# Optimization experiments

Measured on AMD Instinct MI355X. Metric: run time of the kernel, lower is better.

The kernel has to match this reference:

```python
import jax, jax.numpy as jnp
import numpy as np

EPS = 1e-08


def setup_inputs() -> dict:
    key = jax.random.key(0)
    k1, k2 = jax.random.split(key)
    N, D, C = 8192, 512, 1000
    features = jax.random.uniform(k1, (N, D), dtype=jnp.float32)
    logits = jax.random.normal(k2, (N, C), dtype=jnp.float32)
    return {"features": features, "logits": logits}


def reference(features, logits):
    N = features.shape[0]
    # softmax over classes, plus eps (matches F.softmax(...) + eps)
    p = jax.nn.softmax(logits, axis=1) + EPS                     # [N, C]
    # similarity matrix with diagonal removed
    cos_sim = features @ features.T - jnp.eye(N, dtype=features.dtype)  # [N, N]
    neighbor_mask = (cos_sim >= -1).astype(cos_sim.dtype)
    w = cos_sim * neighbor_mask
    w = w / jnp.sum(w, axis=1, keepdims=True)                    # row-normalized weights
    weighted_sum_nb = w @ p                                      # [N, C]
    # F.kl_div(log_input, target, reduction='batchmean')
    # = sum(target * (log(target) - log_input)) / N
    kl = jnp.sum(weighted_sum_nb * (jnp.log(weighted_sum_nb) - jnp.log(p))) / N
    return kl
```

## Files before the change

kernel.cpp:

```cpp
#include <hip/hip_runtime.h>
#include <math.h>

#define NN 8192
#define DD 512
#define CC 1000
#define CP 1024
#define CPD (CP*DD)

typedef __attribute__((ext_vector_type(8))) short short8;
typedef __attribute__((ext_vector_type(4))) float f32x4;
typedef __attribute__((ext_vector_type(4))) unsigned short us4;
typedef __attribute__((ext_vector_type(8))) unsigned short us8;
typedef __attribute__((ext_vector_type(4))) unsigned int ui4;

__device__ __forceinline__ float bf2f(unsigned short u){
  union{unsigned int i; float f;} v; v.i = ((unsigned int)u)<<16; return v.f;
}
__device__ __forceinline__ unsigned short f2bf(float f){
  union{float f; unsigned int i;} v; v.f = f;
  unsigned int r = v.i + 0x7FFF + ((v.i>>16)&1);
  return (unsigned short)(r>>16);
}
__device__ __forceinline__ float waveRedSum(float v){
  #pragma unroll
  for(int o=32;o;o>>=1) v += __shfl_xor(v,o,64);
  return v;
}
__device__ __forceinline__ float waveRedMax(float v){
  #pragma unroll
  for(int o=32;o;o>>=1) v = fmaxf(v,__shfl_xor(v,o,64));
  return v;
}
__device__ __forceinline__ void gload_lds16(const void* g, void* l){
  __builtin_amdgcn_global_load_lds((const __attribute__((address_space(1))) void*)g,
                                   (__attribute__((address_space(3))) void*)l, 16, 0, 0);
}

__global__ __launch_bounds__(256) void k_prep(const float* __restrict__ F,
                                              const float* __restrict__ L,
                                              unsigned short* __restrict__ FbT,
                                              unsigned short* __restrict__ Fb,
                                              float* __restrict__ gpart,
                                              unsigned short* __restrict__ PbT){
  __shared__ __align__(16) char smem[8*1028*4];
  int bid = blockIdx.x;
  int grp = bid/3, r = bid - grp*3;
  int t = threadIdx.x;

  if(r < 2){
    int cb = grp*2 + r;
    unsigned short* lds = (unsigned short*)smem;
    float* gq = (float*)(smem + 64*68*2);
    int i0 = (cb & 127)*64, d0 = (cb >> 7)*64;
    int cx = t&15, ry = t>>4;
    float ca0=0.f,ca1=0.f,ca2=0.f,ca3=0.f;
    #pragma unroll
    for(int rr=0;rr<4;rr++){
      int row = rr*16 + ry;
      f32x4 fv = *(const f32x4*)&F[(size_t)(i0+row)*DD + d0 + cx*4];
      us4 u; u[0]=f2bf(fv[0]); u[1]=f2bf(fv[1]); u[2]=f2bf(fv[2]); u[3]=f2bf(fv[3]);
      *(us4*)&lds[row*68 + cx*4] = u;
      *(us4*)&Fb[(size_t)(i0+row)*DD + d0 + cx*4] = u;
      ca0+=fv[0]; ca1+=fv[1]; ca2+=fv[2]; ca3+=fv[3];
    }
    {
      f32x4 cv; cv[0]=ca0; cv[1]=ca1; cv[2]=ca2; cv[3]=ca3;
      *(f32x4*)&gq[ry*64 + cx*4] = cv;
    }
    __syncthreads();
    #pragma unroll
    for(int rr=0;rr<4;rr++){
      int d = rr*16 + ry;
      us4 u;
      #pragma unroll
      for(int q=0;q<4;q++) u[q] = lds[(cx*4+q)*68 + d];
      *(us4*)&FbT[(size_t)(d0+d)*NN + i0 + cx*4] = u;
    }
    __syncthreads();
    if(t<64){
      float s=0.f;
      #pragma unroll
      for(int j=0;j<16;j++) s += gq[j*64+t];
      gpart[(cb&127)*DD + d0 + t] = s;
    }
  } else {
    int sb = grp;
    unsigned int (*lt)[1028] = (unsigned int(*)[1028])smem;
    int l = t&63, w = t>>6;
    int i0 = sb*16;
    #pragma unroll
    for(int q=0;q<4;q++){
      int rr = w*4 + q;
      int row = i0 + rr;
      const float* lr = L + (size_t)row*CC;
      float v[16]; float mx = -1e30f;
      #pragma unroll
      for(int k=0;k<16;k++){ int c = l + 64*k; v[k] = (c<CC)? lr[c] : -1e30f; mx = fmaxf(mx,v[k]); }
      mx = waveRedMax(mx);
      float s = 0.f;
      #pragma unroll
      for(int k=0;k<16;k++){ v[k] = __expf(v[k]-mx); s += v[k]; }
      s = waveRedSum(s);
      float inv = 1.0f/s;
      #pragma unroll
      for(int k=0;k<16;k++){
        int c = l + 64*k;
        float p = v[k]*inv + 1e-8f;
        unsigned short h = (c<CC)? f2bf(p) : (unsigned short)0;
        *((unsigned short*)&lt[rr>>1][c] + (rr&1)) = h;
      }
    }
    __syncthreads();
    #pragma unroll
    for(int k=0;k<4;k++){
      int c = t + 256*k;
      ui4 a, b;
      #pragma unroll
      for(int j=0;j<4;j++){ a[j] = lt[j][c]; b[j] = lt[j+4][c]; }
      *(ui4*)&PbT[(size_t)c*NN + i0]     = a;
      *(ui4*)&PbT[(size_t)c*NN + i0 + 8] = b;
    }
  }
}

__global__ __launch_bounds__(256,2) void k_gemm1(const unsigned short* __restrict__ A,
                                                 const unsigned short* __restrict__ B,
                                                 unsigned short* __restrict__ Tpb,
                                                 const float* __restrict__ gpart,
                                                 float* __restrict__ g){
  __shared__ unsigned short Al[128*64];
  __shared__ unsigned short Bl[128*64];
  __shared__ float rs[4][64];
  int bid = blockIdx.x;
  int t = threadIdx.x;
  if(bid < 8){
    int d = bid*64 + (t&63);
    int q = t>>6;
    float s = 0.f;
    #pragma unroll
    for(int j=0;j<32;j++) s += gpart[(size_t)(q*32+j)*DD + d];
    rs[q][t&63] = s;
    __syncthreads();
    if(q==0) g[d] = rs[0][t&63]+rs[1][t&63]+rs[2][t&63]+rs[3][t&63];
    return;
  }
  int gb = bid - 8;
  int Lsw = (gb&7)*64 + (gb>>3);
  int l = t&63, w = t>>6;
  int bx = Lsw & 7, by = (Lsw>>3) & 3, bz = Lsw>>5;
  int m0 = bx*128, n0 = by*128;
  int k0 = bz*512;
  int wm = w>>1, wn = w&1;
  f32x4 acc[4][4] = {};
  int srow = w*32 + (l>>3);
  int scl  = (l&7) ^ (srow&7);
  const unsigned short* Ab = A + (size_t)(m0 + srow)*NN + k0 + scl*8;
  const unsigned short* Bb = B + (size_t)(n0 + srow)*NN + k0 + scl*8;
  unsigned short* AlB = Al + (w*32)*64;
  unsigned short* BlB = Bl + (w*32)*64;

  for(int kt=0; kt<512; kt+=64){
    __syncthreads();
    #pragma unroll
    for(int q=0;q<4;q++){
      gload_lds16(Ab + (size_t)q*8*NN + kt, AlB + q*8*64);
      gload_lds16(Bb + (size_t)q*8*NN + kt, BlB + q*8*64);
    }
    asm volatile("s_waitcnt vmcnt(0)" ::: "memory");
    __syncthreads();
    #pragma unroll
    for(int ks=0;ks<2;ks++){
      short8 af[4], bf[4];
      #pragma unroll
      for(int mi=0;mi<4;mi++){
        int rr = wm*64 + mi*16 + (l&15);
        int ch = ((ks<<2) + (l>>4)) ^ (rr&7);
        af[mi] = *(const short8*)&Al[rr*64 + ch*8];
      }
      #pragma unroll
      for(int ni=0;ni<4;ni++){
        int rr = wn*64 + ni*16 + (l&15);
        int ch = ((ks<<2) + (l>>4)) ^ (rr&7);
        bf[ni] = *(const short8*)&Bl[rr*64 + ch*8];
      }
      #pragma unroll
      for(int mi=0;mi<4;mi++)
        #pragma unroll
        for(int ni=0;ni<4;ni++)
          acc[mi][ni] = __builtin_amdgcn_mfma_f32_16x16x32_bf16(af[mi], bf[ni], acc[mi][ni], 0,0,0);
    }
  }
  unsigned short* Tz = Tpb + (size_t)bz*CPD;
  int rbase = (l>>4)*4;
  #pragma unroll
  for(int mi=0;mi<4;mi++){
    int c = m0 + wm*64 + mi*16 + rbase;
    #pragma unroll
    for(int ni=0;ni<4;ni++){
      int d = n0 + wn*64 + ni*16 + (l&15);
      #pragma unroll
      for(int j=0;j<4;j++)
        Tz[(size_t)(c+j)*DD + d] = f2bf(acc[mi][ni][j]);
    }
  }
}

__global__ __launch_bounds__(256) void k_redT(const unsigned short* __restrict__ Tpb,
                                              const unsigned short* __restrict__ Fb,
                                              const float* __restrict__ g,
                                              unsigned short* __restrict__ Ttb,
                                              float* __restrict__ invr){
  int t = threadIdx.x;
  size_t i = ((size_t)blockIdx.x*256 + (size_t)t)*8;
  f32x4 s0 = {0.f,0.f,0.f,0.f}, s1 = {0.f,0.f,0.f,0.f};
  #pragma unroll
  for(int z=0;z<16;z++){
    us8 v = *(const us8*)&Tpb[(size_t)z*CPD + i];
    s0[0]+=bf2f(v[0]); s0[1]+=bf2f(v[1]); s0[2]+=bf2f(v[2]); s0[3]+=bf2f(v[3]);
    s1[0]+=bf2f(v[4]); s1[1]+=bf2f(v[5]); s1[2]+=bf2f(v[6]); s1[3]+=bf2f(v[7]);
  }
  us8 u;
  u[0]=f2bf(s0[0]); u[1]=f2bf(s0[1]); u[2]=f2bf(s0[2]); u[3]=f2bf(s0[3]);
  u[4]=f2bf(s1[0]); u[5]=f2bf(s1[1]); u[6]=f2bf(s1[2]); u[7]=f2bf(s1[3]);
  *(us8*)&Ttb[i] = u;
  int row = blockIdx.x*32 + (t>>3);
  int seg = (t&7)*64;
  const unsigned short* fr = Fb + (size_t)row*DD + seg;
  const float* gr = g + seg;
  float s = 0.f;
  #pragma unroll
  for(int j=0;j<8;j++){
    us8 f8 = *(const us8*)&fr[j*8];
    f32x4 ga = *(const f32x4*)&gr[j*8];
    f32x4 gb = *(const f32x4*)&gr[j*8+4];
    s += bf2f(f8[0])*ga[0]+bf2f(f8[1])*ga[1]+bf2f(f8[2])*ga[2]+bf2f(f8[3])*ga[3]
       + bf2f(f8[4])*gb[0]+bf2f(f8[5])*gb[1]+bf2f(f8[6])*gb[2]+bf2f(f8[7])*gb[3];
  }
  s += __shfl_xor(s,1,64); s += __shfl_xor(s,2,64); s += __shfl_xor(s,4,64);
  if((t&7)==0) invr[row] = 1.0f/(s - 1.0f);
}

__global__ __launch_bounds__(256,2) void k_gemm2(const unsigned short* __restrict__ Fb,
                                                 const unsigned short* __restrict__ Bt,
                                                 const unsigned short* __restrict__ PbT,
                                                 const float* __restrict__ invr,
                                                 float* __restrict__ partials){
  __shared__ __align__(16) unsigned short smem[128*136];
  __shared__ float red[4];
  unsigned short* Al = smem;
  unsigned short* Bl = smem + 128*64;
  int bid = blockIdx.x;
  int Lsw = (bid&7)*64 + (bid>>3);
  int t = threadIdx.x, l = t&63, w = t>>6;
  int m0 = (Lsw>>3)*128, n0 = (Lsw&7)*128;
  int wm = w>>1, wn = w&1;
  f32x4 acc[4][4] = {};
  int srow = w*32 + (l>>3);
  int scl  = (l&7) ^ (srow&7);
  const unsigned short* Ab = Fb + (size_t)(m0 + srow)*DD + scl*8;
  const unsigned short* Bb = Bt + (size_t)(n0 + srow)*DD + scl*8;
  unsigned short* AlB = Al + (w*32)*64;
  unsigned short* BlB = Bl + (w*32)*64;

  for(int kt=0; kt<512; kt+=64){
    __syncthreads();
    #pragma unroll
    for(int q=0;q<4;q++){
      gload_lds16(Ab + (size_t)q*8*DD + kt, AlB + q*8*64);
      gload_lds16(Bb + (size_t)q*8*DD + kt, BlB + q*8*64);
    }
    asm volatile("s_waitcnt vmcnt(0)" ::: "memory");
    __syncthreads();
    #pragma unroll
    for(int ks=0;ks<2;ks++){
      short8 af[4], bf[4];
      #pragma unroll
      for(int mi=0;mi<4;mi++){
        int rr = wm*64 + mi*16 + (l&15);
        int ch = ((ks<<2) + (l>>4)) ^ (rr&7);
        af[mi] = *(const short8*)&Al[rr*64 + ch*8];
      }
      #pragma unroll
      for(int ni=0;ni<4;ni++){
        int rr = wn*64 + ni*16 + (l&15);
        int ch = ((ks<<2) + (l>>4)) ^ (rr&7);
        bf[ni] = *(const short8*)&Bl[rr*64 + ch*8];
      }
      #pragma unroll
      for(int mi=0;mi<4;mi++)
        #pragma unroll
        for(int ni=0;ni<4;ni++)
          acc[mi][ni] = __builtin_amdgcn_mfma_f32_16x16x32_bf16(af[mi], bf[ni], acc[mi][ni], 0,0,0);
    }
  }
  __syncthreads();
  #pragma unroll
  for(int j=0;j<8;j++){
    int e = j*256 + t;
    int row = e >> 4;
    int ch  = e & 15;
    us8 v = *(const us8*)&PbT[(size_t)(n0+row)*NN + m0 + ch*8];
    *(us8*)&smem[row*136 + ch*8] = v;
  }
  __syncthreads();
  float kl = 0.f;
  int rbase = (l>>4)*4;
  #pragma unroll
  for(int mi=0;mi<4;mi++){
    int i_base = m0 + wm*64 + mi*16 + rbase;
    int ci = wm*64 + mi*16 + rbase;
    f32x4 ir4 = *(const f32x4*)&invr[i_base];
    #pragma unroll
    for(int ni=0;ni<4;ni++){
      int cr = wn*64 + ni*16 + (l&15);
      int c = n0 + cr;
      if(c < CC){
        us4 p4 = *(const us4*)&smem[cr*136 + ci];
        #pragma unroll
        for(int j=0;j<4;j++){
          float p = bf2f(p4[j]);
          float ws = (acc[mi][ni][j] - p) * ir4[j];
          kl += ws * (__logf(ws) - __logf(p));
        }
      }
    }
  }
  kl = waveRedSum(kl);
  if(l==0) red[w]=kl;
  __syncthreads();
  if(t==0) partials[Lsw] = red[0]+red[1]+red[2]+red[3];
}

__global__ __launch_bounds__(64) void k_finalize(const float* __restrict__ partials,
                                                 float* __restrict__ out){
  int l = threadIdx.x;
  double s = 0.0;
  for(int j=l; j<512; j+=64) s += (double)partials[j];
  #pragma unroll
  for(int o=32;o;o>>=1) s += __shfl_xor(s,o,64);
  if(l==0) out[0] = (float)(s / (double)NN);
}

extern "C" void kernel_launch(void* const* d_in, const int* in_sizes, int n_in,
                              void* d_out, int out_size, void* d_ws, size_t ws_size,
                              hipStream_t stream){
  const float* F = (const float*)d_in[0];
  const float* L = (const float*)d_in[1];
  float* out = (float*)d_out;

  unsigned char* w8 = (unsigned char*)d_ws;
  unsigned short* FbT = (unsigned short*)w8;
  unsigned short* PbT = (unsigned short*)(w8 + (8u<<20));
  unsigned short* Tpb = (unsigned short*)(w8 + (24u<<20));
  unsigned short* Ttb = (unsigned short*)(w8 + (40u<<20));
  unsigned short* Fb  = (unsigned short*)(w8 + (41u<<20));
  float* gpart        = (float*)(w8 + (49u<<20));
  float* g            = (float*)(w8 + (49u<<20) + 262144);
  float* invr         = (float*)(w8 + (49u<<20) + 264192);
  float* partials     = (float*)(w8 + (49u<<20) + 296960);

  hipLaunchKernelGGL(k_prep,     dim3(1536),   dim3(256), 0, stream, F, L, FbT, Fb, gpart, PbT);
  hipLaunchKernelGGL(k_gemm1,    dim3(520),    dim3(256), 0, stream, PbT, FbT, Tpb, gpart, g);
  hipLaunchKernelGGL(k_redT,     dim3(256),    dim3(256), 0, stream, Tpb, Fb, g, Ttb, invr);
  hipLaunchKernelGGL(k_gemm2,    dim3(512),    dim3(256), 0, stream, Fb, Ttb, PbT, invr, partials);
  hipLaunchKernelGGL(k_finalize, dim3(1),      dim3(64),  0, stream, partials, out);
}
```

Measured before the change: 67.94 us.

## Double-buffer LDS tiles in both GEMM kernels to overlap loads with MFMA

Both GEMM kernels now use two LDS buffers and prefetch the next K tile from global memory into the spare buffer while MFMAs run on the current one. A partial vmcnt wait lets the current tile's loads complete while the next tile's loads stay in flight. This is meant to hide global-to-LDS latency that the old load-wait-compute loop exposed. LDS use per block doubles to 64KB, which may limit occupancy under launch_bounds(256,2), and the raw s_barrier calls without lgkmcnt waits carry a risk of ordering hazards.

```diff
diff --git a/kernel.cpp b/kernel.cpp
--- a/kernel.cpp
+++ b/kernel.cpp
@@ -128,8 +128,7 @@
                                                  unsigned short* __restrict__ Tpb,
                                                  const float* __restrict__ gpart,
                                                  float* __restrict__ g){
-  __shared__ unsigned short Al[128*64];
-  __shared__ unsigned short Bl[128*64];
+  __shared__ __align__(16) unsigned short smem[4*8192];
   __shared__ float rs[4][64];
   int bid = blockIdx.x;
   int t = threadIdx.x;
@@ -156,18 +155,30 @@
   int scl  = (l&7) ^ (srow&7);
   const unsigned short* Ab = A + (size_t)(m0 + srow)*NN + k0 + scl*8;
   const unsigned short* Bb = B + (size_t)(n0 + srow)*NN + k0 + scl*8;
-  unsigned short* AlB = Al + (w*32)*64;
-  unsigned short* BlB = Bl + (w*32)*64;
-
+  int ldsOff = (w*32)*64;
+
+  #pragma unroll
+  for(int q=0;q<4;q++){
+    gload_lds16(Ab + (size_t)q*8*NN, smem + ldsOff + q*8*64);
+    gload_lds16(Bb + (size_t)q*8*NN, smem + 8192 + ldsOff + q*8*64);
+  }
+  int cur = 0;
   for(int kt=0; kt<512; kt+=64){
-    __syncthreads();
-    #pragma unroll
-    for(int q=0;q<4;q++){
-      gload_lds16(Ab + (size_t)q*8*NN + kt, AlB + q*8*64);
-      gload_lds16(Bb + (size_t)q*8*NN + kt, BlB + q*8*64);
-    }
-    asm volatile("s_waitcnt vmcnt(0)" ::: "memory");
-    __syncthreads();
+    if(kt+64 < 512){
+      unsigned short* An = smem + (cur^1)*16384 + ldsOff;
+      unsigned short* Bn = smem + (cur^1)*16384 + 8192 + ldsOff;
+      #pragma unroll
+      for(int q=0;q<4;q++){
+        gload_lds16(Ab + (size_t)q*8*NN + kt + 64, An + q*8*64);
+        gload_lds16(Bb + (size_t)q*8*NN + kt + 64, Bn + q*8*64);
+      }
+      asm volatile("s_waitcnt vmcnt(8)" ::: "memory");
+    } else {
+      asm volatile("s_waitcnt vmcnt(0)" ::: "memory");
+    }
+    __builtin_amdgcn_s_barrier();
+    const unsigned short* Ac = smem + cur*16384;
+    const unsigned short* Bc = smem + cur*16384 + 8192;
     #pragma unroll
     for(int ks=0;ks<2;ks++){
       short8 af[4], bf[4];
@@ -175,13 +186,13 @@
       for(int mi=0;mi<4;mi++){
         int rr = wm*64 + mi*16 + (l&15);
         int ch = ((ks<<2) + (l>>4)) ^ (rr&7);
-        af[mi] = *(const short8*)&Al[rr*64 + ch*8];
+        af[mi] = *(const short8*)&Ac[rr*64 + ch*8];
       }
       #pragma unroll
       for(int ni=0;ni<4;ni++){
         int rr = wn*64 + ni*16 + (l&15);
         int ch = ((ks<<2) + (l>>4)) ^ (rr&7);
-        bf[ni] = *(const short8*)&Bl[rr*64 + ch*8];
+        bf[ni] = *(const short8*)&Bc[rr*64 + ch*8];
       }
       #pragma unroll
       for(int mi=0;mi<4;mi++)
@@ -189,6 +200,8 @@
         for(int ni=0;ni<4;ni++)
           acc[mi][ni] = __builtin_amdgcn_mfma_f32_16x16x32_bf16(af[mi], bf[ni], acc[mi][ni], 0,0,0);
     }
+    __builtin_amdgcn_s_barrier();
+    cur ^= 1;
   }
   unsigned short* Tz = Tpb + (size_t)bz*CPD;
   int rbase = (l>>4)*4;
@@ -245,10 +258,8 @@
                                                  const unsigned short* __restrict__ PbT,
                                                  const float* __restrict__ invr,
                                                  float* __restrict__ partials){
-  __shared__ __align__(16) unsigned short smem[128*136];
+  __shared__ __align__(16) unsigned short smem[4*8192];
   __shared__ float red[4];
-  unsigned short* Al = smem;
-  unsigned short* Bl = smem + 128*64;
   int bid = blockIdx.x;
   int Lsw = (bid&7)*64 + (bid>>3);
   int t = threadIdx.x, l = t&63, w = t>>6;
@@ -259,18 +270,30 @@
   int scl  = (l&7) ^ (srow&7);
   const unsigned short* Ab = Fb + (size_t)(m0 + srow)*DD + scl*8;
   const unsigned short* Bb = Bt + (size_t)(n0 + srow)*DD + scl*8;
-  unsigned short* AlB = Al + (w*32)*64;
-  unsigned short* BlB = Bl + (w*32)*64;
-
+  int ldsOff = (w*32)*64;
+
+  #pragma unroll
+  for(int q=0;q<4;q++){
+    gload_lds16(Ab + (size_t)q*8*DD, smem + ldsOff + q*8*64);
+    gload_lds16(Bb + (size_t)q*8*DD, smem + 8192 + ldsOff + q*8*64);
+  }
+  int cur = 0;
   for(int kt=0; kt<512; kt+=64){
-    __syncthreads();
-    #pragma unroll
-    for(int q=0;q<4;q++){
-      gload_lds16(Ab + (size_t)q*8*DD + kt, AlB + q*8*64);
-      gload_lds16(Bb + (size_t)q*8*DD + kt, BlB + q*8*64);
-    }
-    asm volatile("s_waitcnt vmcnt(0)" ::: "memory");
-    __syncthreads();
+    if(kt+64 < 512){
+      unsigned short* An = smem + (cur^1)*16384 + ldsOff;
+      unsigned short* Bn = smem + (cur^1)*16384 + 8192 + ldsOff;
+      #pragma unroll
+      for(int q=0;q<4;q++){
+        gload_lds16(Ab + (size_t)q*8*DD + kt + 64, An + q*8*64);
+        gload_lds16(Bb + (size_t)q*8*DD + kt + 64, Bn + q*8*64);
+      }
+      asm volatile("s_waitcnt vmcnt(8)" ::: "memory");
+    } else {
+      asm volatile("s_waitcnt vmcnt(0)" ::: "memory");
+    }
+    __builtin_amdgcn_s_barrier();
+    const unsigned short* Ac = smem + cur*16384;
+    const unsigned short* Bc = smem + cur*16384 + 8192;
     #pragma unroll
     for(int ks=0;ks<2;ks++){
       short8 af[4], bf[4];
@@ -278,13 +301,13 @@
       for(int mi=0;mi<4;mi++){
         int rr = wm*64 + mi*16 + (l&15);
         int ch = ((ks<<2) + (l>>4)) ^ (rr&7);
-        af[mi] = *(const short8*)&Al[rr*64 + ch*8];
+        af[mi] = *(const short8*)&Ac[rr*64 + ch*8];
       }
       #pragma unroll
       for(int ni=0;ni<4;ni++){
         int rr = wn*64 + ni*16 + (l&15);
         int ch = ((ks<<2) + (l>>4)) ^ (rr&7);
-        bf[ni] = *(const short8*)&Bl[rr*64 + ch*8];
+        bf[ni] = *(const short8*)&Bc[rr*64 + ch*8];
       }
       #pragma unroll
       for(int mi=0;mi<4;mi++)
@@ -292,6 +315,8 @@
         for(int ni=0;ni<4;ni++)
           acc[mi][ni] = __builtin_amdgcn_mfma_f32_16x16x32_bf16(af[mi], bf[ni], acc[mi][ni], 0,0,0);
     }
+    __builtin_amdgcn_s_barrier();
+    cur ^= 1;
   }
   __syncthreads();
   #pragma unroll
```

New measurement: 66.55 us. 1.02x faster.
